# Kernel tuning notes

Measured on AMD Instinct MI355X. Metric: run time of the kernel, lower is better.

## Reference

```python
import jax, jax.numpy as jnp
import numpy as np

B, L, H2 = 8, 512, 512  # batch, seq len (shared by a/b/c), 2*hidden


def setup_inputs() -> dict:
    key = jax.random.key(0)
    ka, kb, kc, kw1, kw2, kw3 = jax.random.split(key, 6)
    enc_a = jax.random.normal(ka, (B, L, H2), dtype=jnp.float32)
    enc_b = jax.random.normal(kb, (B, L, H2), dtype=jnp.float32)
    enc_c = jax.random.normal(kc, (B, L, H2), dtype=jnp.float32)
    # nn.Linear(6h, 1, bias=False) weight vectors; scaled so softmax isn't saturated
    w_ab = jax.random.normal(kw1, (3 * H2,), dtype=jnp.float32) * 0.02
    w_ac = jax.random.normal(kw2, (3 * H2,), dtype=jnp.float32) * 0.02
    w_bc = jax.random.normal(kw3, (3 * H2,), dtype=jnp.float32) * 0.02
    return {"encoded_a": enc_a, "encoded_b": enc_b, "encoded_c": enc_c,
            "w_ab": w_ab, "w_ac": w_ac, "w_bc": w_bc}


def _pair_att(A, Bx, w):
    """BiDAF-style pair attention.
    Original: S[b,i,j] = w . cat(A_i, B_j, A_i*B_j); here decomposed as
    S = A@w1 + B@w2 + A diag(w3) B^T  (identical math, no (B,La,Lb,6h) tensor).
    Returns a2b (B,La,2h) and b2a (B,2h) [pre-repeat].
    """
    h2 = A.shape[-1]
    wA, wB, wM = w[:h2], w[h2:2 * h2], w[2 * h2:]
    S = (A @ wA)[:, :, None] + (Bx @ wB)[:, None, :] \
        + jnp.einsum('bik,bjk->bij', A * wM, Bx)          # (B, La, Lb)
    a2b = jnp.einsum('bij,bjd->bid', jax.nn.softmax(S, axis=-1), Bx)  # (B, La, 2h)
    beta = jax.nn.softmax(jnp.max(S, axis=2), axis=-1)                # (B, La)
    b2a = jnp.einsum('bi,bid->bd', beta, A)                           # (B, 2h)
    return a2b, b2a


def reference(encoded_a, encoded_b, encoded_c, w_ab, w_ac, w_bc):
    b, len_b = encoded_b.shape[0], encoded_b.shape[1]
    len_c = encoded_c.shape[1]
    a2b, b2a = _pair_att(encoded_a, encoded_b, w_ab)
    a2c, c2a = _pair_att(encoded_a, encoded_c, w_ac)
    b2c, c2b = _pair_att(encoded_b, encoded_c, w_bc)
    # repeat the pooled vectors along the target sequence dim (as in torch .repeat)
    b2a = jnp.broadcast_to(b2a[:, None, :], (b, len_b, b2a.shape[-1]))
    c2a = jnp.broadcast_to(c2a[:, None, :], (b, len_c, c2a.shape[-1]))
    c2b = jnp.broadcast_to(c2b[:, None, :], (b, len_c, c2b.shape[-1]))
    att_a = jnp.concatenate((encoded_a, a2b, a2c, encoded_a * a2b, encoded_a * a2c), axis=2)
    att_b = jnp.concatenate((encoded_b, b2a, b2c, encoded_b * b2a, encoded_b * b2c), axis=2)
    att_c = jnp.concatenate((encoded_c, c2a, c2b, encoded_c * c2a, encoded_c * c2b), axis=2)
    return jnp.concatenate((att_a, att_b, att_c), axis=1)  # (B, La+Lb+Lc, 10h)
```

## Files before the change

kernel.cpp:

```cpp
#include <hip/hip_runtime.h>
#include <cmath>

#define BB 8
#define LL 512
#define HH 512

typedef __attribute__((ext_vector_type(8))) short short8;
typedef __attribute__((ext_vector_type(4))) float floatx4;

#define MM __builtin_amdgcn_mfma_f32_16x16x32_bf16
#define SB() __builtin_amdgcn_sched_barrier(0)

__device__ __forceinline__ unsigned short f2bf(float x) {
  unsigned int u = __float_as_uint(x);
  unsigned int r = (u + 0x7fffu + ((u >> 16) & 1u)) >> 16;
  return (unsigned short)r;
}

__global__ __launch_bounds__(256) void kP1(
    const float* __restrict__ A, const float* __restrict__ Bm, const float* __restrict__ C,
    const float* __restrict__ w0, const float* __restrict__ w1, const float* __restrict__ w2,
    unsigned short* __restrict__ Xm0, unsigned short* __restrict__ Xm1,
    unsigned short* __restrict__ Xm2,
    unsigned short* __restrict__ Bn, unsigned short* __restrict__ Cn,
    float* __restrict__ rowterm, float* __restrict__ colterm) {
  int tid = threadIdx.x;
  int wave = blockIdx.x * 4 + (tid >> 6);
  int lane = tid & 63;
  int m = wave >> 12;
  int rem = wave & 4095;
  int b = rem >> 9, i = rem & 511;
  const float* src = (m == 0) ? A : (m == 1 ? Bm : C);
  const float* rp = src + (size_t)rem * HH + lane * 8;
  float4 xa = *(const float4*)rp, xb = *(const float4*)(rp + 4);
  float x[8] = {xa.x, xa.y, xa.z, xa.w, xb.x, xb.y, xb.z, xb.w};

  const float *wva, *wvb;
  float *da, *db;
  if (m == 0) {
    wva = w0;      wvb = w1;
    da = rowterm + (0 * BB + b) * LL + i;  db = rowterm + (1 * BB + b) * LL + i;
  } else if (m == 1) {
    wva = w0 + HH; wvb = w2;
    da = colterm + (0 * BB + b) * LL + i;  db = rowterm + (2 * BB + b) * LL + i;
  } else {
    wva = w1 + HH; wvb = w2 + HH;
    da = colterm + (1 * BB + b) * LL + i;  db = colterm + (2 * BB + b) * LL + i;
  }
  const float* ap1 = wva + lane * 8;
  const float* bp1 = wvb + lane * 8;
  float4 wa1 = *(const float4*)ap1, wa2 = *(const float4*)(ap1 + 4);
  float4 wb1 = *(const float4*)bp1, wb2 = *(const float4*)(bp1 + 4);
  float wa[8] = {wa1.x, wa1.y, wa1.z, wa1.w, wa2.x, wa2.y, wa2.z, wa2.w};
  float wb[8] = {wb1.x, wb1.y, wb1.z, wb1.w, wb2.x, wb2.y, wb2.z, wb2.w};
  float a1 = 0.f, a2 = 0.f;
#pragma unroll
  for (int e = 0; e < 8; ++e) { a1 += x[e] * wa[e]; a2 += x[e] * wb[e]; }
#pragma unroll
  for (int off = 32; off; off >>= 1) {
    a1 += __shfl_xor(a1, off, 64);
    a2 += __shfl_xor(a2, off, 64);
  }
  if (lane == 0) { *da = a1; *db = a2; }

  size_t oo = (size_t)rem * HH + lane * 8;
  if (m == 0) {
    const float* m0 = w0 + 2 * HH + lane * 8;
    const float* m1 = w1 + 2 * HH + lane * 8;
    float4 ma1 = *(const float4*)m0, ma2 = *(const float4*)(m0 + 4);
    float4 mb1 = *(const float4*)m1, mb2 = *(const float4*)(m1 + 4);
    float wm0[8] = {ma1.x, ma1.y, ma1.z, ma1.w, ma2.x, ma2.y, ma2.z, ma2.w};
    float wm1[8] = {mb1.x, mb1.y, mb1.z, mb1.w, mb2.x, mb2.y, mb2.z, mb2.w};
    short8 o0, o1;
#pragma unroll
    for (int e = 0; e < 8; ++e) { o0[e] = (short)f2bf(x[e] * wm0[e]); o1[e] = (short)f2bf(x[e] * wm1[e]); }
    *(short8*)(Xm0 + oo) = o0;
    *(short8*)(Xm1 + oo) = o1;
  } else if (m == 1) {
    const float* m2 = w2 + 2 * HH + lane * 8;
    float4 mc1 = *(const float4*)m2, mc2 = *(const float4*)(m2 + 4);
    float wm2[8] = {mc1.x, mc1.y, mc1.z, mc1.w, mc2.x, mc2.y, mc2.z, mc2.w};
    short8 on, o2;
#pragma unroll
    for (int e = 0; e < 8; ++e) { on[e] = (short)f2bf(x[e]); o2[e] = (short)f2bf(x[e] * wm2[e]); }
    *(short8*)(Bn + oo) = on;
    *(short8*)(Xm2 + oo) = o2;
  } else {
    short8 on;
#pragma unroll
    for (int e = 0; e < 8; ++e) on[e] = (short)f2bf(x[e]);
    *(short8*)(Cn + oo) = on;
  }
}

__global__ __launch_bounds__(256) void k0t(
    const unsigned short* __restrict__ Bn, const unsigned short* __restrict__ Cn,
    unsigned short* __restrict__ Bt, unsigned short* __restrict__ Ct) {
  __shared__ unsigned short tile[64][68];
  int bid = blockIdx.x;
  int s = bid >> 9;
  int rem = bid & 511;
  int b = rem >> 6, tr = (rem >> 3) & 7, tc = rem & 7;
  const unsigned short* src = s ? Cn : Bn;
  unsigned short* dt = s ? Ct : Bt;
  int t = threadIdx.x;
#pragma unroll
  for (int h = 0; h < 2; ++h) {
    int id = h * 256 + t;
    int row = id >> 3, c8 = id & 7;
    short8 v = *(const short8*)(src + ((size_t)(b * 512 + tr * 64 + row)) * 512 + tc * 64 + c8 * 8);
    *(short8*)&tile[row][c8 * 8] = v;
  }
  __syncthreads();
  int d = t >> 2, jc = t & 3;
  short8 v0, v1;
#pragma unroll
  for (int e = 0; e < 8; ++e) v0[e] = (short)tile[jc * 16 + e][d];
#pragma unroll
  for (int e = 0; e < 8; ++e) v1[e] = (short)tile[jc * 16 + 8 + e][d];
  unsigned short* tp = dt + ((size_t)(b * 512 + tc * 64 + d)) * 512 + tr * 64 + jc * 16;
  *(short8*)tp = v0;
  *(short8*)(tp + 8) = v1;
}

__global__ __launch_bounds__(512, 2) void k2_mfma(
    const unsigned short* __restrict__ Xm0, const unsigned short* __restrict__ Xm1,
    const unsigned short* __restrict__ Xm2,
    const unsigned short* __restrict__ Bn, const unsigned short* __restrict__ Cn,
    const unsigned short* __restrict__ Bt, const unsigned short* __restrict__ Ct,
    const float* __restrict__ A, const float* __restrict__ Bm,
    const float* __restrict__ rowterm, const float* __restrict__ colterm,
    float* __restrict__ mrow, float* __restrict__ out) {
  __shared__ __align__(16) unsigned char smem[65536];
  unsigned short* A_lds = (unsigned short*)smem;
  unsigned short* P_lds = (unsigned short*)smem;
  float* sm_m = (float*)smem;
  float* sm_l = (float*)(smem + 2048);

  int tid = threadIdx.x;
  int bid0 = blockIdx.x;
  int bid = (bid0 & 7) * 24 + (bid0 >> 3);
  int p = bid >> 6;
  int b = (bid >> 3) & 7;
  int rb = bid & 7;
  int i0 = rb * 64;

  const unsigned short* Xmp = (p == 0) ? Xm0 : ((p == 1) ? Xm1 : Xm2);
  const unsigned short* Yn  = (p == 0) ? Bn : Cn;
  const unsigned short* Yt  = (p == 0) ? Bt : Ct;
  const float* X = (p == 2) ? Bm : A;

  int wc = tid >> 6;
  int lane = tid & 63;
  int n16 = lane & 15, q = lane >> 4;
  int e8 = n16 & 7;

#pragma unroll
  for (int j = 0; j < 8; ++j) {
    int idx = j * 512 + tid;
    int row = idx >> 6;
    int cc = idx & 63;
    short8 v = *(const short8*)(Xmp + ((size_t)(b * LL + i0 + row)) * HH + cc * 8);
    *(short8*)&A_lds[row * 512 + (cc ^ (row & 7)) * 8] = v;
  }
  __syncthreads();

  const unsigned short* br0 = Yn + ((size_t)(b * LL + wc * 64 + n16)) * HH + q * 8;
  const unsigned short* br1 = br0 + 16 * HH;
  const unsigned short* br2 = br0 + 32 * HH;
  const unsigned short* br3 = br0 + 48 * HH;

  floatx4 acc[4][4] = {};
  short8 Ax0[4], Ax1[4], Bx0[4], Bx1[4], Bx2[4];

#define LA(AF, kk) do { int ch_ = (((kk) * 4 + q) ^ e8) * 8; \
    AF[0] = *(const short8*)&A_lds[(n16)      * 512 + ch_]; \
    AF[1] = *(const short8*)&A_lds[(16 + n16) * 512 + ch_]; \
    AF[2] = *(const short8*)&A_lds[(32 + n16) * 512 + ch_]; \
    AF[3] = *(const short8*)&A_lds[(48 + n16) * 512 + ch_]; } while (0)
#define LB1(BF, kk) do { const int k0_ = (kk) * 32; \
    BF[0] = *(const short8*)(br0 + k0_); \
    BF[1] = *(const short8*)(br1 + k0_); \
    BF[2] = *(const short8*)(br2 + k0_); \
    BF[3] = *(const short8*)(br3 + k0_); } while (0)
#define MF1(AF, BF) do { \
    acc[0][0]=MM(AF[0],BF[0],acc[0][0],0,0,0); acc[0][1]=MM(AF[0],BF[1],acc[0][1],0,0,0); \
    acc[0][2]=MM(AF[0],BF[2],acc[0][2],0,0,0); acc[0][3]=MM(AF[0],BF[3],acc[0][3],0,0,0); \
    acc[1][0]=MM(AF[1],BF[0],acc[1][0],0,0,0); acc[1][1]=MM(AF[1],BF[1],acc[1][1],0,0,0); \
    acc[1][2]=MM(AF[1],BF[2],acc[1][2],0,0,0); acc[1][3]=MM(AF[1],BF[3],acc[1][3],0,0,0); \
    acc[2][0]=MM(AF[2],BF[0],acc[2][0],0,0,0); acc[2][1]=MM(AF[2],BF[1],acc[2][1],0,0,0); \
    acc[2][2]=MM(AF[2],BF[2],acc[2][2],0,0,0); acc[2][3]=MM(AF[2],BF[3],acc[2][3],0,0,0); \
    acc[3][0]=MM(AF[3],BF[0],acc[3][0],0,0,0); acc[3][1]=MM(AF[3],BF[1],acc[3][1],0,0,0); \
    acc[3][2]=MM(AF[3],BF[2],acc[3][2],0,0,0); acc[3][3]=MM(AF[3],BF[3],acc[3][3],0,0,0); } while (0)

  LB1(Bx0, 0); LB1(Bx1, 1); LB1(Bx2, 2); LA(Ax0, 0); LA(Ax1, 1); SB();
  MF1(Ax0, Bx0); LA(Ax0, 2);  LB1(Bx0, 3);  SB();
  MF1(Ax1, Bx1); LA(Ax1, 3);  LB1(Bx1, 4);  SB();
  MF1(Ax0, Bx2); LA(Ax0, 4);  LB1(Bx2, 5);  SB();
  MF1(Ax1, Bx0); LA(Ax1, 5);  LB1(Bx0, 6);  SB();
  MF1(Ax0, Bx1); LA(Ax0, 6);  LB1(Bx1, 7);  SB();
  MF1(Ax1, Bx2); LA(Ax1, 7);  LB1(Bx2, 8);  SB();
  MF1(Ax0, Bx0); LA(Ax0, 8);  LB1(Bx0, 9);  SB();
  MF1(Ax1, Bx1); LA(Ax1, 9);  LB1(Bx1, 10); SB();
  MF1(Ax0, Bx2); LA(Ax0, 10); LB1(Bx2, 11); SB();
  MF1(Ax1, Bx0); LA(Ax1, 11); LB1(Bx0, 12); SB();
  MF1(Ax0, Bx1); LA(Ax0, 12); LB1(Bx1, 13); SB();
  MF1(Ax1, Bx2); LA(Ax1, 13); LB1(Bx2, 14); SB();
  MF1(Ax0, Bx0); LA(Ax0, 14); LB1(Bx0, 15); SB();
  MF1(Ax1, Bx1); LA(Ax1, 15); SB();
  MF1(Ax0, Bx2); SB();
  MF1(Ax1, Bx0);
#undef LA
#undef LB1
#undef MF1

  __syncthreads();

  float rtv[4][4], ctv[4], mh[4][4], ml[4][4], rinv[4][4];
  {
    const float* rtp = rowterm + (p * BB + b) * LL + i0 + q * 4;
#pragma unroll
    for (int rt = 0; rt < 4; ++rt)
#pragma unroll
      for (int r = 0; r < 4; ++r) rtv[rt][r] = rtp[rt * 16 + r];
    const float* ctp = colterm + (p * BB + b) * LL + wc * 64 + n16;
#pragma unroll
    for (int f = 0; f < 4; ++f) ctv[f] = ctp[f * 16];
  }
#pragma unroll
  for (int rt = 0; rt < 4; ++rt)
#pragma unroll
    for (int r = 0; r < 4; ++r) {
      float m = -1e30f;
#pragma unroll
      for (int f = 0; f < 4; ++f) {
        float v = acc[rt][f][r] + rtv[rt][r] + ctv[f];
        acc[rt][f][r] = v;
        m = fmaxf(m, v);
      }
      m = fmaxf(m, __shfl_xor(m, 1, 64));
      m = fmaxf(m, __shfl_xor(m, 2, 64));
      m = fmaxf(m, __shfl_xor(m, 4, 64));
      m = fmaxf(m, __shfl_xor(m, 8, 64));
      mh[rt][r] = m;
    }
  if (n16 == 0) {
#pragma unroll
    for (int rt = 0; rt < 4; ++rt)
#pragma unroll
      for (int r = 0; r < 4; ++r) sm_m[wc * 64 + rt * 16 + q * 4 + r] = mh[rt][r];
  }
  __syncthreads();
#pragma unroll
  for (int rt = 0; rt < 4; ++rt)
#pragma unroll
    for (int r = 0; r < 4; ++r) {
      float m = mh[rt][r];
#pragma unroll
      for (int k = 0; k < 8; ++k) m = fmaxf(m, sm_m[k * 64 + rt * 16 + q * 4 + r]);
      mh[rt][r] = m;
      float l = 0.f;
#pragma unroll
      for (int f = 0; f < 4; ++f) {
        float pv = __expf(acc[rt][f][r] - m);
        acc[rt][f][r] = pv;
        l += pv;
      }
      l += __shfl_xor(l, 1, 64);
      l += __shfl_xor(l, 2, 64);
      l += __shfl_xor(l, 4, 64);
      l += __shfl_xor(l, 8, 64);
      ml[rt][r] = l;
    }
  if (n16 == 0) {
#pragma unroll
    for (int rt = 0; rt < 4; ++rt)
#pragma unroll
      for (int r = 0; r < 4; ++r) sm_l[wc * 64 + rt * 16 + q * 4 + r] = ml[rt][r];
    if (wc == 0) {
#pragma unroll
      for (int rt = 0; rt < 4; ++rt)
#pragma unroll
        for (int r = 0; r < 4; ++r)
          mrow[(p * BB + b) * LL + i0 + rt * 16 + q * 4 + r] = mh[rt][r];
    }
  }
  __syncthreads();
#pragma unroll
  for (int rt = 0; rt < 4; ++rt)
#pragma unroll
    for (int r = 0; r < 4; ++r) {
      float lf = 0.f;
#pragma unroll
      for (int k = 0; k < 8; ++k) lf += sm_l[k * 64 + rt * 16 + q * 4 + r];
      rinv[rt][r] = 1.f / lf;
    }
  __syncthreads();

#pragma unroll
  for (int f = 0; f < 4; ++f) {
    int c = wc * 8 + f * 2 + (n16 >> 3);
#pragma unroll
    for (int rt = 0; rt < 4; ++rt)
#pragma unroll
      for (int r = 0; r < 4; ++r) {
        int row = rt * 16 + q * 4 + r;
        int pc = c ^ (row & 7);
        P_lds[row * 512 + pc * 8 + e8] = f2bf(acc[rt][f][r]);
      }
  }
  __syncthreads();

  const unsigned short* tr0 = Yt + ((size_t)(b * LL + wc * 64 + n16)) * HH + q * 8;
  const unsigned short* tr1 = tr0 + 16 * HH;
  const unsigned short* tr2 = tr0 + 32 * HH;
  const unsigned short* tr3 = tr0 + 48 * HH;

  floatx4 oacc[4][4] = {};
  short8 Px0[4], Px1[4], By0[4], By1[4], By2[4];

#define LP(PF, kj) do { int ch_ = (((kj) * 4 + q) ^ e8) * 8; \
    PF[0] = *(const short8*)&P_lds[(n16)      * 512 + ch_]; \
    PF[1] = *(const short8*)&P_lds[(16 + n16) * 512 + ch_]; \
    PF[2] = *(const short8*)&P_lds[(32 + n16) * 512 + ch_]; \
    PF[3] = *(const short8*)&P_lds[(48 + n16) * 512 + ch_]; } while (0)
#define LB2(BF, kj) do { const int j0_ = (kj) * 32; \
    BF[0] = *(const short8*)(tr0 + j0_); \
    BF[1] = *(const short8*)(tr1 + j0_); \
    BF[2] = *(const short8*)(tr2 + j0_); \
    BF[3] = *(const short8*)(tr3 + j0_); } while (0)
#define MF2(PF, BF) do { \
    oacc[0][0]=MM(PF[0],BF[0],oacc[0][0],0,0,0); oacc[0][1]=MM(PF[0],BF[1],oacc[0][1],0,0,0); \
    oacc[0][2]=MM(PF[0],BF[2],oacc[0][2],0,0,0); oacc[0][3]=MM(PF[0],BF[3],oacc[0][3],0,0,0); \
    oacc[1][0]=MM(PF[1],BF[0],oacc[1][0],0,0,0); oacc[1][1]=MM(PF[1],BF[1],oacc[1][1],0,0,0); \
    oacc[1][2]=MM(PF[1],BF[2],oacc[1][2],0,0,0); oacc[1][3]=MM(PF[1],BF[3],oacc[1][3],0,0,0); \
    oacc[2][0]=MM(PF[2],BF[0],oacc[2][0],0,0,0); oacc[2][1]=MM(PF[2],BF[1],oacc[2][1],0,0,0); \
    oacc[2][2]=MM(PF[2],BF[2],oacc[2][2],0,0,0); oacc[2][3]=MM(PF[2],BF[3],oacc[2][3],0,0,0); \
    oacc[3][0]=MM(PF[3],BF[0],oacc[3][0],0,0,0); oacc[3][1]=MM(PF[3],BF[1],oacc[3][1],0,0,0); \
    oacc[3][2]=MM(PF[3],BF[2],oacc[3][2],0,0,0); oacc[3][3]=MM(PF[3],BF[3],oacc[3][3],0,0,0); } while (0)

  LB2(By0, 0); LB2(By1, 1); LB2(By2, 2); LP(Px0, 0); LP(Px1, 1); SB();
  MF2(Px0, By0); LP(Px0, 2);  LB2(By0, 3);  SB();
  MF2(Px1, By1); LP(Px1, 3);  LB2(By1, 4);  SB();
  MF2(Px0, By2); LP(Px0, 4);  LB2(By2, 5);  SB();
  MF2(Px1, By0); LP(Px1, 5);  LB2(By0, 6);  SB();
  MF2(Px0, By1); LP(Px0, 6);  LB2(By1, 7);  SB();
  MF2(Px1, By2); LP(Px1, 7);  LB2(By2, 8);  SB();
  MF2(Px0, By0); LP(Px0, 8);  LB2(By0, 9);  SB();
  MF2(Px1, By1); LP(Px1, 9);  LB2(By1, 10); SB();
  MF2(Px0, By2); LP(Px0, 10); LB2(By2, 11); SB();
  MF2(Px1, By0); LP(Px1, 11); LB2(By0, 12); SB();
  MF2(Px0, By1); LP(Px0, 12); LB2(By1, 13); SB();
  MF2(Px1, By2); LP(Px1, 13); LB2(By2, 14); SB();
  MF2(Px0, By0); LP(Px0, 14); LB2(By0, 15); SB();
  MF2(Px1, By1); LP(Px1, 15); SB();
  MF2(Px0, By2); SB();
  MF2(Px1, By0);
#undef LP
#undef LB2
#undef MF2

  int secoff, colbase;
  if      (p == 0) { secoff = 0;   colbase = 512;  }
  else if (p == 1) { secoff = 0;   colbase = 1024; }
  else             { secoff = 512; colbase = 1024; }

#pragma unroll
  for (int f = 0; f < 4; ++f) {
    int d = wc * 64 + f * 16 + n16;
#pragma unroll
    for (int rt = 0; rt < 4; ++rt)
#pragma unroll
      for (int r = 0; r < 4; ++r) {
        int ig = i0 + rt * 16 + q * 4 + r;
        float val = oacc[rt][f][r] * rinv[rt][r];
        size_t ob = ((size_t)b * 1536 + secoff + ig) * 2560;
        out[ob + colbase + d] = val;
        out[ob + colbase + 1024 + d] = X[((size_t)b * LL + ig) * HH + d] * val;
      }
  }
}

__global__ __launch_bounds__(512) void k3_beta(
    const float* __restrict__ A, const float* __restrict__ Bm,
    const float* __restrict__ mrow, float* __restrict__ vvec) {
  __shared__ float red[512];
  __shared__ float beta[LL];
  __shared__ float s_inv;
  int blk = blockIdx.x;
  int p = blk >> 6;
  int rem2 = blk & 63;
  int b = rem2 >> 3;
  int dch = rem2 & 7;
  int tid = threadIdx.x;
  const float* m = mrow + (p * BB + b) * LL;
  red[tid] = m[tid];
  __syncthreads();
  for (int off = 256; off; off >>= 1) {
    if (tid < off) red[tid] = fmaxf(red[tid], red[tid + off]);
    __syncthreads();
  }
  float mx = red[0];
  __syncthreads();
  float e0 = __expf(m[tid] - mx);
  beta[tid] = e0;
  red[tid] = e0;
  __syncthreads();
  for (int off = 256; off; off >>= 1) {
    if (tid < off) red[tid] += red[tid + off];
    __syncthreads();
  }
  if (tid == 0) s_inv = 1.f / red[0];
  __syncthreads();
  const float* Xb = ((p == 2) ? Bm : A) + (size_t)b * LL * HH;
  int d = dch * 64 + (tid & 63);
  int ig = tid >> 6;
  float acc = 0.f;
#pragma unroll 4
  for (int i2 = ig * 64; i2 < ig * 64 + 64; ++i2)
    acc += beta[i2] * Xb[(size_t)i2 * HH + d];
  red[tid] = acc;
  __syncthreads();
  if (tid < 64) {
    float s = 0.f;
#pragma unroll
    for (int k = 0; k < 8; ++k) s += red[tid + k * 64];
    vvec[(p * BB + b) * HH + dch * 64 + tid] = s * s_inv;
  }
}

__global__ __launch_bounds__(256) void k4_finalize(
    const float* __restrict__ A, const float* __restrict__ Bm, const float* __restrict__ C,
    const float* __restrict__ vvec, float* __restrict__ out) {
  unsigned int idx = blockIdx.x * 256 + threadIdx.x;
  int f4 = idx & 127;
  int i  = (idx >> 7) & 511;
  unsigned int ub = idx >> 16;
  unsigned int u = ub % 9;
  unsigned int b = ub / 9;
  int sec, slice;
  if (u == 0)      { sec = 0; slice = 0; }
  else if (u <= 3) { sec = 1; slice = (u == 1) ? 0 : (u == 2 ? 1 : 3); }
  else             { sec = 2; slice = (int)u - 4; }
  int cc = f4 * 4;
  const float* enc = sec == 0 ? A : (sec == 1 ? Bm : C);
  float4 val;
  if (slice == 0) {
    val = *(const float4*)(enc + ((size_t)b * LL + i) * HH + cc);
  } else {
    int vp = (sec == 1) ? 0 : ((slice == 1 || slice == 3) ? 1 : 2);
    float4 v = *(const float4*)(vvec + (vp * BB + b) * HH + cc);
    if (slice <= 2) {
      val = v;
    } else {
      float4 e = *(const float4*)(enc + ((size_t)b * LL + i) * HH + cc);
      val.x = e.x * v.x; val.y = e.y * v.y; val.z = e.z * v.z; val.w = e.w * v.w;
    }
  }
  *(float4*)(out + ((size_t)b * 1536 + sec * 512 + i) * 2560 + slice * 512 + cc) = val;
}

extern "C" void kernel_launch(void* const* d_in, const int* in_sizes, int n_in,
                              void* d_out, int out_size, void* d_ws, size_t ws_size,
                              hipStream_t stream) {
  const float* A  = (const float*)d_in[0];
  const float* Bm = (const float*)d_in[1];
  const float* C  = (const float*)d_in[2];
  const float* w0 = (const float*)d_in[3];
  const float* w1 = (const float*)d_in[4];
  const float* w2 = (const float*)d_in[5];
  float* out = (float*)d_out;

  float* wsf = (float*)d_ws;
  float* rowterm = wsf;
  float* colterm = wsf + 12288;
  float* mrow    = wsf + 24576;
  float* vvec    = wsf + 36864;
  unsigned short* wss = (unsigned short*)(wsf + 49152);
  const size_t MSZ = (size_t)BB * LL * HH;
  unsigned short* Bn  = wss;
  unsigned short* Cn  = wss + MSZ;
  unsigned short* Bt  = wss + 2 * MSZ;
  unsigned short* Ct  = wss + 3 * MSZ;
  unsigned short* Xm0 = wss + 4 * MSZ;
  unsigned short* Xm1 = wss + 5 * MSZ;
  unsigned short* Xm2 = wss + 6 * MSZ;

  kP1<<<3072, 256, 0, stream>>>(A, Bm, C, w0, w1, w2, Xm0, Xm1, Xm2, Bn, Cn,
                                rowterm, colterm);
  k0t<<<1024, 256, 0, stream>>>(Bn, Cn, Bt, Ct);
  k2_mfma<<<192, 512, 0, stream>>>(Xm0, Xm1, Xm2, Bn, Cn, Bt, Ct, A, Bm,
                                   rowterm, colterm, mrow, out);
  k3_beta<<<192, 512, 0, stream>>>(A, Bm, mrow, vvec);
  k4_finalize<<<18432, 256, 0, stream>>>(A, Bm, C, vvec, out);
}
```

Before: 216.5 us.

## Fuse bf16 prep and transpose into one kernel; deepen MFMA B-prefetch to four stages

```diff
diff --git a/kernel.cpp b/kernel.cpp
--- a/kernel.cpp
+++ b/kernel.cpp
@@ -17,110 +17,125 @@
   return (unsigned short)r;
 }
 
-__global__ __launch_bounds__(256) void kP1(
+__global__ __launch_bounds__(512) void kP2(
     const float* __restrict__ A, const float* __restrict__ Bm, const float* __restrict__ C,
     const float* __restrict__ w0, const float* __restrict__ w1, const float* __restrict__ w2,
     unsigned short* __restrict__ Xm0, unsigned short* __restrict__ Xm1,
     unsigned short* __restrict__ Xm2,
     unsigned short* __restrict__ Bn, unsigned short* __restrict__ Cn,
+    unsigned short* __restrict__ Bt, unsigned short* __restrict__ Ct,
     float* __restrict__ rowterm, float* __restrict__ colterm) {
+  __shared__ unsigned short tile[8][64][64];
+
+  int bid = blockIdx.x;
+  int m = bid >> 6;
+  int rem = bid & 63;
+  int b = rem >> 3, rb = rem & 7;
+  int i0 = rb * 64;
   int tid = threadIdx.x;
-  int wave = blockIdx.x * 4 + (tid >> 6);
+  int w = tid >> 6;
   int lane = tid & 63;
-  int m = wave >> 12;
-  int rem = wave & 4095;
-  int b = rem >> 9, i = rem & 511;
+
   const float* src = (m == 0) ? A : (m == 1 ? Bm : C);
-  const float* rp = src + (size_t)rem * HH + lane * 8;
-  float4 xa = *(const float4*)rp, xb = *(const float4*)(rp + 4);
-  float x[8] = {xa.x, xa.y, xa.z, xa.w, xb.x, xb.y, xb.z, xb.w};
-
   const float *wva, *wvb;
   float *da, *db;
   if (m == 0) {
     wva = w0;      wvb = w1;
-    da = rowterm + (0 * BB + b) * LL + i;  db = rowterm + (1 * BB + b) * LL + i;
+    da = rowterm + (0 * BB + b) * LL;  db = rowterm + (1 * BB + b) * LL;
   } else if (m == 1) {
     wva = w0 + HH; wvb = w2;
-    da = colterm + (0 * BB + b) * LL + i;  db = rowterm + (2 * BB + b) * LL + i;
+    da = colterm + (0 * BB + b) * LL;  db = rowterm + (2 * BB + b) * LL;
   } else {
     wva = w1 + HH; wvb = w2 + HH;
-    da = colterm + (1 * BB + b) * LL + i;  db = colterm + (2 * BB + b) * LL + i;
-  }
-  const float* ap1 = wva + lane * 8;
-  const float* bp1 = wvb + lane * 8;
-  float4 wa1 = *(const float4*)ap1, wa2 = *(const float4*)(ap1 + 4);
-  float4 wb1 = *(const float4*)bp1, wb2 = *(const float4*)(bp1 + 4);
-  float wa[8] = {wa1.x, wa1.y, wa1.z, wa1.w, wa2.x, wa2.y, wa2.z, wa2.w};
-  float wb[8] = {wb1.x, wb1.y, wb1.z, wb1.w, wb2.x, wb2.y, wb2.z, wb2.w};
-  float a1 = 0.f, a2 = 0.f;
-#pragma unroll
-  for (int e = 0; e < 8; ++e) { a1 += x[e] * wa[e]; a2 += x[e] * wb[e]; }
-#pragma unroll
-  for (int off = 32; off; off >>= 1) {
-    a1 += __shfl_xor(a1, off, 64);
-    a2 += __shfl_xor(a2, off, 64);
-  }
-  if (lane == 0) { *da = a1; *db = a2; }
-
-  size_t oo = (size_t)rem * HH + lane * 8;
+    da = colterm + (1 * BB + b) * LL;  db = colterm + (2 * BB + b) * LL;
+  }
+
+  float wa[8], wb[8], wmA[8], wmB[8];
+  {
+    const float* ap1 = wva + lane * 8;
+    const float* bp1 = wvb + lane * 8;
+    float4 t0 = *(const float4*)ap1, t1 = *(const float4*)(ap1 + 4);
+    float4 t2 = *(const float4*)bp1, t3 = *(const float4*)(bp1 + 4);
+    wa[0]=t0.x; wa[1]=t0.y; wa[2]=t0.z; wa[3]=t0.w; wa[4]=t1.x; wa[5]=t1.y; wa[6]=t1.z; wa[7]=t1.w;
+    wb[0]=t2.x; wb[1]=t2.y; wb[2]=t2.z; wb[3]=t2.w; wb[4]=t3.x; wb[5]=t3.y; wb[6]=t3.z; wb[7]=t3.w;
+  }
   if (m == 0) {
     const float* m0 = w0 + 2 * HH + lane * 8;
     const float* m1 = w1 + 2 * HH + lane * 8;
-    float4 ma1 = *(const float4*)m0, ma2 = *(const float4*)(m0 + 4);
-    float4 mb1 = *(const float4*)m1, mb2 = *(const float4*)(m1 + 4);
-    float wm0[8] = {ma1.x, ma1.y, ma1.z, ma1.w, ma2.x, ma2.y, ma2.z, ma2.w};
-    float wm1[8] = {mb1.x, mb1.y, mb1.z, mb1.w, mb2.x, mb2.y, mb2.z, mb2.w};
-    short8 o0, o1;
-#pragma unroll
-    for (int e = 0; e < 8; ++e) { o0[e] = (short)f2bf(x[e] * wm0[e]); o1[e] = (short)f2bf(x[e] * wm1[e]); }
-    *(short8*)(Xm0 + oo) = o0;
-    *(short8*)(Xm1 + oo) = o1;
+    float4 t0 = *(const float4*)m0, t1 = *(const float4*)(m0 + 4);
+    float4 t2 = *(const float4*)m1, t3 = *(const float4*)(m1 + 4);
+    wmA[0]=t0.x; wmA[1]=t0.y; wmA[2]=t0.z; wmA[3]=t0.w; wmA[4]=t1.x; wmA[5]=t1.y; wmA[6]=t1.z; wmA[7]=t1.w;
+    wmB[0]=t2.x; wmB[1]=t2.y; wmB[2]=t2.z; wmB[3]=t2.w; wmB[4]=t3.x; wmB[5]=t3.y; wmB[6]=t3.z; wmB[7]=t3.w;
   } else if (m == 1) {
     const float* m2 = w2 + 2 * HH + lane * 8;
-    float4 mc1 = *(const float4*)m2, mc2 = *(const float4*)(m2 + 4);
-    float wm2[8] = {mc1.x, mc1.y, mc1.z, mc1.w, mc2.x, mc2.y, mc2.z, mc2.w};
-    short8 on, o2;
-#pragma unroll
-    for (int e = 0; e < 8; ++e) { on[e] = (short)f2bf(x[e]); o2[e] = (short)f2bf(x[e] * wm2[e]); }
-    *(short8*)(Bn + oo) = on;
-    *(short8*)(Xm2 + oo) = o2;
-  } else {
-    short8 on;
-#pragma unroll
-    for (int e = 0; e < 8; ++e) on[e] = (short)f2bf(x[e]);
-    *(short8*)(Cn + oo) = on;
-  }
-}
-
-__global__ __launch_bounds__(256) void k0t(
-    const unsigned short* __restrict__ Bn, const unsigned short* __restrict__ Cn,
-    unsigned short* __restrict__ Bt, unsigned short* __restrict__ Ct) {
-  __shared__ unsigned short tile[64][68];
-  int bid = blockIdx.x;
-  int s = bid >> 9;
-  int rem = bid & 511;
-  int b = rem >> 6, tr = (rem >> 3) & 7, tc = rem & 7;
-  const unsigned short* src = s ? Cn : Bn;
-  unsigned short* dt = s ? Ct : Bt;
-  int t = threadIdx.x;
-#pragma unroll
-  for (int h = 0; h < 2; ++h) {
-    int id = h * 256 + t;
-    int row = id >> 3, c8 = id & 7;
-    short8 v = *(const short8*)(src + ((size_t)(b * 512 + tr * 64 + row)) * 512 + tc * 64 + c8 * 8);
-    *(short8*)&tile[row][c8 * 8] = v;
-  }
-  __syncthreads();
-  int d = t >> 2, jc = t & 3;
-  short8 v0, v1;
-#pragma unroll
-  for (int e = 0; e < 8; ++e) v0[e] = (short)tile[jc * 16 + e][d];
-#pragma unroll
-  for (int e = 0; e < 8; ++e) v1[e] = (short)tile[jc * 16 + 8 + e][d];
-  unsigned short* tp = dt + ((size_t)(b * 512 + tc * 64 + d)) * 512 + tr * 64 + jc * 16;
-  *(short8*)tp = v0;
-  *(short8*)(tp + 8) = v1;
+    float4 t0 = *(const float4*)m2, t1 = *(const float4*)(m2 + 4);
+    wmA[0]=t0.x; wmA[1]=t0.y; wmA[2]=t0.z; wmA[3]=t0.w; wmA[4]=t1.x; wmA[5]=t1.y; wmA[6]=t1.z; wmA[7]=t1.w;
+  }
+
+  int tc = lane >> 3, c8 = lane & 7;
+
+#pragma unroll 2
+  for (int rr = 0; rr < 8; ++rr) {
+    int ro = w * 8 + rr;
+    int i = i0 + ro;
+    const float* rp = src + ((size_t)(b * 512 + i)) * HH + lane * 8;
+    float4 xa = *(const float4*)rp, xb = *(const float4*)(rp + 4);
+    float x[8] = {xa.x, xa.y, xa.z, xa.w, xb.x, xb.y, xb.z, xb.w};
+
+    float a1 = 0.f, a2 = 0.f;
+#pragma unroll
+    for (int e = 0; e < 8; ++e) { a1 += x[e] * wa[e]; a2 += x[e] * wb[e]; }
+#pragma unroll
+    for (int off = 32; off; off >>= 1) {
+      a1 += __shfl_xor(a1, off, 64);
+      a2 += __shfl_xor(a2, off, 64);
+    }
+    if (lane == 0) { da[i] = a1; db[i] = a2; }
+
+    size_t oo = ((size_t)(b * 512 + i)) * HH + lane * 8;
+    if (m == 0) {
+      short8 o0, o1;
+#pragma unroll
+      for (int e = 0; e < 8; ++e) { o0[e] = (short)f2bf(x[e] * wmA[e]); o1[e] = (short)f2bf(x[e] * wmB[e]); }
+      *(short8*)(Xm0 + oo) = o0;
+      *(short8*)(Xm1 + oo) = o1;
+    } else if (m == 1) {
+      short8 on, o2;
+#pragma unroll
+      for (int e = 0; e < 8; ++e) { on[e] = (short)f2bf(x[e]); o2[e] = (short)f2bf(x[e] * wmA[e]); }
+      *(short8*)(Bn + oo) = on;
+      *(short8*)(Xm2 + oo) = o2;
+      *(short8*)&tile[tc][ro][(c8 ^ (ro & 7)) * 8] = on;
+    } else {
+      short8 on;
+#pragma unroll
+      for (int e = 0; e < 8; ++e) on[e] = (short)f2bf(x[e]);
+      *(short8*)(Cn + oo) = on;
+      *(short8*)&tile[tc][ro][(c8 ^ (ro & 7)) * 8] = on;
+    }
+  }
+
+  if (m >= 1) {
+    __syncthreads();
+    unsigned short* dt = (m == 1) ? Bt : Ct;
+    int tsub = tid >> 8;
+    int tt = tid & 255;
+    int d = tt >> 2, jc = tt & 3;
+#pragma unroll
+    for (int p2 = 0; p2 < 4; ++p2) {
+      int tcs = p2 * 2 + tsub;
+      short8 v0, v1;
+#pragma unroll
+      for (int e = 0; e < 8; ++e)
+        v0[e] = (short)tile[tcs][jc * 16 + e][((d >> 3) ^ e) * 8 + (d & 7)];
+#pragma unroll
+      for (int e = 0; e < 8; ++e)
+        v1[e] = (short)tile[tcs][jc * 16 + 8 + e][((d >> 3) ^ e) * 8 + (d & 7)];
+      unsigned short* tp = dt + ((size_t)(b * 512 + tcs * 64 + d)) * 512 + i0 + jc * 16;
+      *(short8*)tp = v0;
+      *(short8*)(tp + 8) = v1;
+    }
+  }
 }
 
 __global__ __launch_bounds__(512, 2) void k2_mfma(
@@ -171,7 +186,7 @@
   const unsigned short* br3 = br0 + 48 * HH;
 
   floatx4 acc[4][4] = {};
-  short8 Ax0[4], Ax1[4], Bx0[4], Bx1[4], Bx2[4];
+  short8 Ax0[4], Ax1[4], Bx0[4], Bx1[4], Bx2[4], Bx3[4];
 
 #define LA(AF, kk) do { int ch_ = (((kk) * 4 + q) ^ e8) * 8; \
     AF[0] = *(const short8*)&A_lds[(n16)      * 512 + ch_]; \
@@ -193,23 +208,23 @@
     acc[3][0]=MM(AF[3],BF[0],acc[3][0],0,0,0); acc[3][1]=MM(AF[3],BF[1],acc[3][1],0,0,0); \
     acc[3][2]=MM(AF[3],BF[2],acc[3][2],0,0,0); acc[3][3]=MM(AF[3],BF[3],acc[3][3],0,0,0); } while (0)
 
-  LB1(Bx0, 0); LB1(Bx1, 1); LB1(Bx2, 2); LA(Ax0, 0); LA(Ax1, 1); SB();
-  MF1(Ax0, Bx0); LA(Ax0, 2);  LB1(Bx0, 3);  SB();
-  MF1(Ax1, Bx1); LA(Ax1, 3);  LB1(Bx1, 4);  SB();
-  MF1(Ax0, Bx2); LA(Ax0, 4);  LB1(Bx2, 5);  SB();
-  MF1(Ax1, Bx0); LA(Ax1, 5);  LB1(Bx0, 6);  SB();
-  MF1(Ax0, Bx1); LA(Ax0, 6);  LB1(Bx1, 7);  SB();
-  MF1(Ax1, Bx2); LA(Ax1, 7);  LB1(Bx2, 8);  SB();
-  MF1(Ax0, Bx0); LA(Ax0, 8);  LB1(Bx0, 9);  SB();
-  MF1(Ax1, Bx1); LA(Ax1, 9);  LB1(Bx1, 10); SB();
-  MF1(Ax0, Bx2); LA(Ax0, 10); LB1(Bx2, 11); SB();
-  MF1(Ax1, Bx0); LA(Ax1, 11); LB1(Bx0, 12); SB();
-  MF1(Ax0, Bx1); LA(Ax0, 12); LB1(Bx1, 13); SB();
-  MF1(Ax1, Bx2); LA(Ax1, 13); LB1(Bx2, 14); SB();
-  MF1(Ax0, Bx0); LA(Ax0, 14); LB1(Bx0, 15); SB();
+  LB1(Bx0, 0); LB1(Bx1, 1); LB1(Bx2, 2); LB1(Bx3, 3); LA(Ax0, 0); LA(Ax1, 1); SB();
+  MF1(Ax0, Bx0); LA(Ax0, 2);  LB1(Bx0, 4);  SB();
+  MF1(Ax1, Bx1); LA(Ax1, 3);  LB1(Bx1, 5);  SB();
+  MF1(Ax0, Bx2); LA(Ax0, 4);  LB1(Bx2, 6);  SB();
+  MF1(Ax1, Bx3); LA(Ax1, 5);  LB1(Bx3, 7);  SB();
+  MF1(Ax0, Bx0); LA(Ax0, 6);  LB1(Bx0, 8);  SB();
+  MF1(Ax1, Bx1); LA(Ax1, 7);  LB1(Bx1, 9);  SB();
+  MF1(Ax0, Bx2); LA(Ax0, 8);  LB1(Bx2, 10); SB();
+  MF1(Ax1, Bx3); LA(Ax1, 9);  LB1(Bx3, 11); SB();
+  MF1(Ax0, Bx0); LA(Ax0, 10); LB1(Bx0, 12); SB();
+  MF1(Ax1, Bx1); LA(Ax1, 11); LB1(Bx1, 13); SB();
+  MF1(Ax0, Bx2); LA(Ax0, 12); LB1(Bx2, 14); SB();
+  MF1(Ax1, Bx3); LA(Ax1, 13); LB1(Bx3, 15); SB();
+  MF1(Ax0, Bx0); LA(Ax0, 14); SB();
   MF1(Ax1, Bx1); LA(Ax1, 15); SB();
   MF1(Ax0, Bx2); SB();
-  MF1(Ax1, Bx0);
+  MF1(Ax1, Bx3);
 #undef LA
 #undef LB1
 #undef MF1
@@ -317,7 +332,7 @@
   const unsigned short* tr3 = tr0 + 48 * HH;
 
   floatx4 oacc[4][4] = {};
-  short8 Px0[4], Px1[4], By0[4], By1[4], By2[4];
+  short8 Px0[4], Px1[4], By0[4], By1[4], By2[4], By3[4];
 
 #define LP(PF, kj) do { int ch_ = (((kj) * 4 + q) ^ e8) * 8; \
     PF[0] = *(const short8*)&P_lds[(n16)      * 512 + ch_]; \
@@ -339,23 +354,23 @@
     oacc[3][0]=MM(PF[3],BF[0],oacc[3][0],0,0,0); oacc[3][1]=MM(PF[3],BF[1],oacc[3][1],0,0,0); \
     oacc[3][2]=MM(PF[3],BF[2],oacc[3][2],0,0,0); oacc[3][3]=MM(PF[3],BF[3],oacc[3][3],0,0,0); } while (0)
 
-  LB2(By0, 0); LB2(By1, 1); LB2(By2, 2); LP(Px0, 0); LP(Px1, 1); SB();
-  MF2(Px0, By0); LP(Px0, 2);  LB2(By0, 3);  SB();
-  MF2(Px1, By1); LP(Px1, 3);  LB2(By1, 4);  SB();
-  MF2(Px0, By2); LP(Px0, 4);  LB2(By2, 5);  SB();
-  MF2(Px1, By0); LP(Px1, 5);  LB2(By0, 6);  SB();
-  MF2(Px0, By1); LP(Px0, 6);  LB2(By1, 7);  SB();
-  MF2(Px1, By2); LP(Px1, 7);  LB2(By2, 8);  SB();
-  MF2(Px0, By0); LP(Px0, 8);  LB2(By0, 9);  SB();
-  MF2(Px1, By1); LP(Px1, 9);  LB2(By1, 10); SB();
-  MF2(Px0, By2); LP(Px0, 10); LB2(By2, 11); SB();
-  MF2(Px1, By0); LP(Px1, 11); LB2(By0, 12); SB();
-  MF2(Px0, By1); LP(Px0, 12); LB2(By1, 13); SB();
-  MF2(Px1, By2); LP(Px1, 13); LB2(By2, 14); SB();
-  MF2(Px0, By0); LP(Px0, 14); LB2(By0, 15); SB();
+  LB2(By0, 0); LB2(By1, 1); LB2(By2, 2); LB2(By3, 3); LP(Px0, 0); LP(Px1, 1); SB();
+  MF2(Px0, By0); LP(Px0, 2);  LB2(By0, 4);  SB();
+  MF2(Px1, By1); LP(Px1, 3);  LB2(By1, 5);  SB();
+  MF2(Px0, By2); LP(Px0, 4);  LB2(By2, 6);  SB();
+  MF2(Px1, By3); LP(Px1, 5);  LB2(By3, 7);  SB();
+  MF2(Px0, By0); LP(Px0, 6);  LB2(By0, 8);  SB();
+  MF2(Px1, By1); LP(Px1, 7);  LB2(By1, 9);  SB();
+  MF2(Px0, By2); LP(Px0, 8);  LB2(By2, 10); SB();
+  MF2(Px1, By3); LP(Px1, 9);  LB2(By3, 11); SB();
+  MF2(Px0, By0); LP(Px0, 10); LB2(By0, 12); SB();
+  MF2(Px1, By1); LP(Px1, 11); LB2(By1, 13); SB();
+  MF2(Px0, By2); LP(Px0, 12); LB2(By2, 14); SB();
+  MF2(Px1, By3); LP(Px1, 13); LB2(By3, 15); SB();
+  MF2(Px0, By0); LP(Px0, 14); SB();
   MF2(Px1, By1); LP(Px1, 15); SB();
   MF2(Px0, By2); SB();
-  MF2(Px1, By0);
+  MF2(Px1, By3);
 #undef LP
 #undef LB2
 #undef MF2
@@ -486,9 +501,8 @@
   unsigned short* Xm1 = wss + 5 * MSZ;
   unsigned short* Xm2 = wss + 6 * MSZ;
 
-  kP1<<<3072, 256, 0, stream>>>(A, Bm, C, w0, w1, w2, Xm0, Xm1, Xm2, Bn, Cn,
-                                rowterm, colterm);
-  k0t<<<1024, 256, 0, stream>>>(Bn, Cn, Bt, Ct);
+  kP2<<<192, 512, 0, stream>>>(A, Bm, C, w0, w1, w2, Xm0, Xm1, Xm2, Bn, Cn,
+                               Bt, Ct, rowterm, colterm);
   k2_mfma<<<192, 512, 0, stream>>>(Xm0, Xm1, Xm2, Bn, Cn, Bt, Ct, A, Bm,
                                    rowterm, colterm, mrow, out);
   k3_beta<<<192, 512, 0, stream>>>(A, Bm, mrow, vvec);
```

New measurement: 214.6 us. Within noise of the previous version (-0.9%).
